# Kernel tuning notes

Measured on AMD Instinct MI355X. Metric: run time of the kernel, lower is better.

The kernel has to match this reference:

```python
import jax, jax.numpy as jnp
import numpy as np

BN_EPS = 1e-5

def _bn(h, gamma, beta):
    # training-mode BatchNorm1d over node dim, biased variance (as torch)
    m = jnp.mean(h, axis=0)
    v = jnp.var(h, axis=0)
    return (h - m) * jax.lax.rsqrt(v + BN_EPS) * gamma + beta

def _gin(x, edge_index, W, b, n_nodes):
    # PyG GINConv (eps=0): h = Linear(x + sum_{j in N(i)} x_j)
    src, dst = edge_index[0], edge_index[1]
    agg = jax.ops.segment_sum(x[src], dst, num_segments=n_nodes)
    return (x + agg) @ W + b

def setup_inputs() -> dict:
    key = jax.random.key(0)
    ks = jax.random.split(key, 16)
    N, E, D, H, G = 50000, 800000, 128, 256, 64
    x = jax.random.normal(ks[0], (N, D), dtype=jnp.float32)
    edge_index = jax.random.randint(ks[1], (2, E), 0, N, dtype=jnp.int64)
    batch = jnp.sort(jax.random.randint(ks[2], (N,), 0, G, dtype=jnp.int64))
    s = 0.05
    return {
        "x": x, "edge_index": edge_index, "batch": batch, "num_graphs": G,
        "W1": jax.random.normal(ks[3], (D, H), jnp.float32) * s,
        "b1": jnp.zeros((H,), jnp.float32),
        "W2": jax.random.normal(ks[4], (H, H), jnp.float32) * s,
        "b2": jnp.zeros((H,), jnp.float32),
        "W3": jax.random.normal(ks[5], (H, H), jnp.float32) * s,
        "b3": jnp.zeros((H,), jnp.float32),
        "g1": jnp.ones((H,), jnp.float32), "be1": jnp.zeros((H,), jnp.float32),
        "g2": jnp.ones((H,), jnp.float32), "be2": jnp.zeros((H,), jnp.float32),
        "g3": jnp.ones((H,), jnp.float32), "be3": jnp.zeros((H,), jnp.float32),
        "fcW1": jax.random.normal(ks[6], (H, H), jnp.float32) * s,
        "fcb1": jnp.zeros((H,), jnp.float32),
        "fcW2": jax.random.normal(ks[7], (H, 1), jnp.float32) * s,
        "fcb2": jnp.zeros((1,), jnp.float32),
    }

def reference(x, edge_index, batch, num_graphs, W1, b1, W2, b2, W3, b3,
              g1, be1, g2, be2, g3, be3, fcW1, fcb1, fcW2, fcb2):
    n_nodes = x.shape[0]
    # dropout treated as identity (eval / deterministic)
    x1 = jax.nn.relu(_bn(_gin(x, edge_index, W1, b1, n_nodes), g1, be1))
    x2 = jax.nn.relu(_bn(_gin(x1, edge_index, W2, b2, n_nodes), g2, be2)) + x1
    x3 = jax.nn.relu(_bn(_gin(x2, edge_index, W3, b3, n_nodes), g3, be3)) + x2
    # global mean pool over graphs
    sums = jax.ops.segment_sum(x3, batch, num_segments=num_graphs)
    cnt = jax.ops.segment_sum(jnp.ones((n_nodes,), x3.dtype), batch, num_segments=num_graphs)
    pooled = sums / jnp.maximum(cnt, 1.0)[:, None]
    h = jax.nn.relu(pooled @ fcW1 + fcb1)
    return h @ fcW2 + fcb2
```

## Files before the change

### kernel.cpp

```cpp
#include <hip/hip_runtime.h>
#include <hip/hip_bf16.h>
#include <stdint.h>

#define HDIM 256
#define NGRAPH 64

typedef short s16x8 __attribute__((ext_vector_type(8)));
typedef float f32x4 __attribute__((ext_vector_type(4)));

__device__ __forceinline__ float bf2f(unsigned short u){
    union { unsigned int i; float f; } x; x.i = ((unsigned int)u) << 16; return x.f;
}
__device__ __forceinline__ unsigned short f2bf(float f){
    union { float f; unsigned int i; } x; x.f = f;
    unsigned int r = x.i + 0x7fffu + ((x.i >> 16) & 1u);
    return (unsigned short)(r >> 16);
}
__device__ __forceinline__ float ldf(const void* p, int i, int f32){
    return f32 ? ((const float*)p)[i] : bf2f(((const unsigned short*)p)[i]);
}

__global__ void zero_detect_kernel(int* __restrict__ p, int n,
                                   const unsigned short* __restrict__ x,
                                   const int* __restrict__ ei, const int* __restrict__ batch,
                                   int E, int N, int* __restrict__ flags){
    int i = blockIdx.x * 256 + threadIdx.x;
    if (i < n) p[i] = 0;
    if (i == 0){
        int c = 0;
        for (int k = 0; k < 128; k++){
            unsigned e = (x[2 * k] >> 7) & 0xFFu;
            if (e >= 100u && e <= 140u) c++;
        }
        flags[0] = (c < 96) ? 1 : 0;
        int z = (ei[2*E - 1] == 0) && (ei[2*E - 3] == 0) && (ei[2*E - 5] == 0) && (ei[2*E - 7] == 0);
        flags[1] = z ? 1 : 0;
        flags[2] = (batch[N - 1] == 0) ? 1 : 0;
    }
}

__global__ void hist_kernel(const int* __restrict__ ei, int E, int N,
                            const int* __restrict__ flags, int* __restrict__ deg){
    int e = blockIdx.x * 256 + threadIdx.x;
    if (e < E){
        int is64 = flags[1];
        int d = is64 ? ei[2 * E + 2 * e] : ei[E + e];
        if ((unsigned)d < (unsigned)N) atomicAdd(&deg[d], 1);
    }
}

__global__ void scan1_kernel(const int* __restrict__ deg, int N,
                             int* __restrict__ incl, int* __restrict__ bsums){
    __shared__ int sm[256];
    int t = threadIdx.x;
    int i = blockIdx.x * 256 + t;
    int v = (i < N) ? deg[i] : 0;
    sm[t] = v; __syncthreads();
    for (int off = 1; off < 256; off <<= 1){
        int tv = (t >= off) ? sm[t - off] : 0;
        __syncthreads();
        sm[t] += tv;
        __syncthreads();
    }
    if (i < N) incl[i] = sm[t];
    if (t == 255) bsums[blockIdx.x] = sm[255];
}

__global__ void scan23_kernel(const int* __restrict__ deg, int N, int E, int nb,
                              const int* __restrict__ bsums, int* __restrict__ rowptr){
    __shared__ int sm[256];
    int t = threadIdx.x;
    int bid = blockIdx.x;
    sm[t] = (t < nb && t < bid) ? bsums[t] : 0;
    __syncthreads();
    for (int s = 128; s > 0; s >>= 1){
        if (t < s) sm[t] += sm[t + s];
        __syncthreads();
    }
    int prefix = sm[0];
    int i = bid * 256 + t;
    if (i < N) rowptr[i] = rowptr[i] - deg[i] + prefix;
    if (i == 0) rowptr[N] = E;
}

__global__ void fill_kernel(const int* __restrict__ ei, int E, int N,
                            const int* __restrict__ flags,
                            const int* __restrict__ rowptr, int* __restrict__ fillc,
                            int* __restrict__ csr){
    int e = blockIdx.x * 256 + threadIdx.x;
    if (e < E){
        int is64 = flags[1];
        int d = is64 ? ei[2 * E + 2 * e] : ei[E + e];
        int s = is64 ? ei[2 * e]         : ei[e];
        if ((unsigned)d < (unsigned)N){
            int p = atomicAdd(&fillc[d], 1);
            csr[rowptr[d] + p] = s;
        }
    }
}

__global__ void prep_kernel(const void* __restrict__ W1, unsigned short* __restrict__ Wt1,
                            const void* __restrict__ W2, unsigned short* __restrict__ Wt2,
                            const void* __restrict__ W3, unsigned short* __restrict__ Wt3,
                            const void* __restrict__ x, unsigned short* __restrict__ Xc,
                            int nx8, const int* __restrict__ flags){
    int bid = blockIdx.x;
    int f32 = flags[0];
    if (bid < 640){
        const void* W; unsigned short* Wt; int K, base;
        if (bid < 128)      { W = W1; Wt = Wt1; K = 128; base = bid; }
        else if (bid < 384) { W = W2; Wt = Wt2; K = 256; base = bid - 128; }
        else                { W = W3; Wt = Wt3; K = 256; base = bid - 384; }
        int idx = base * 256 + threadIdx.x;
        int n = idx / K, k = idx - n * K;
        Wt[idx] = f2bf(ldf(W, k * 256 + n, f32));
    } else {
        int i = (bid - 640) * 256 + threadIdx.x;
        if (i >= nx8) return;
        int base = i * 8;
        unsigned short o[8];
        if (f32){
            const float* s = (const float*)x + base;
            float4 a = *(const float4*)s;
            float4 b = *(const float4*)(s + 4);
            o[0]=f2bf(a.x); o[1]=f2bf(a.y); o[2]=f2bf(a.z); o[3]=f2bf(a.w);
            o[4]=f2bf(b.x); o[5]=f2bf(b.y); o[6]=f2bf(b.z); o[7]=f2bf(b.w);
        } else {
            *(uint4*)o = *(const uint4*)((const unsigned short*)x + base);
        }
        *(uint4*)&Xc[base] = *(uint4*)o;
    }
}

template<int C>
__global__ __launch_bounds__(256) void agg_vec(const unsigned short* __restrict__ feat, int ldi,
                                               const int* __restrict__ rowptr, const int* __restrict__ csr,
                                               unsigned short* __restrict__ Y, int ldo, int N){
    constexpr int L   = C / 8;
    constexpr int NPB = 256 / L;
    int node = blockIdx.x * NPB + threadIdx.x / L;
    int lane = threadIdx.x & (L - 1);
    if (node >= N) return;
    int c0 = lane * 8;
    const unsigned short* base = feat + c0;

    unsigned short t0[8];
    *(uint4*)t0 = *(const uint4*)&feat[(size_t)node * ldi + c0];
    float acc[8];
    #pragma unroll
    for (int j = 0; j < 8; j++) acc[j] = bf2f(t0[j]);

    int lo = rowptr[node], hi = rowptr[node + 1];
    int e = lo;
    for (; e + 3 < hi; e += 4){
        int s0 = csr[e], s1 = csr[e + 1], s2 = csr[e + 2], s3 = csr[e + 3];
        unsigned short ta[8], tb[8], tc[8], td[8];
        *(uint4*)ta = *(const uint4*)&base[(size_t)s0 * ldi];
        *(uint4*)tb = *(const uint4*)&base[(size_t)s1 * ldi];
        *(uint4*)tc = *(const uint4*)&base[(size_t)s2 * ldi];
        *(uint4*)td = *(const uint4*)&base[(size_t)s3 * ldi];
        #pragma unroll
        for (int j = 0; j < 8; j++)
            acc[j] += (bf2f(ta[j]) + bf2f(tb[j])) + (bf2f(tc[j]) + bf2f(td[j]));
    }
    for (; e < hi; e++){
        int s0 = csr[e];
        unsigned short ta[8];
        *(uint4*)ta = *(const uint4*)&base[(size_t)s0 * ldi];
        #pragma unroll
        for (int j = 0; j < 8; j++) acc[j] += bf2f(ta[j]);
    }
    unsigned short o[8];
    #pragma unroll
    for (int j = 0; j < 8; j++) o[j] = f2bf(acc[j]);
    *(uint4*)&Y[(size_t)node * ldo + c0] = *(uint4*)o;
}

__global__ __launch_bounds__(256) void gemm_tile(
    unsigned short* __restrict__ AC, int K,
    const unsigned short* __restrict__ Bt, const void* __restrict__ bias,
    int M, const int* __restrict__ flags,
    float* __restrict__ S, float* __restrict__ Q)
{
    __shared__ __align__(16) unsigned short As[64 * 72];
    __shared__ __align__(16) unsigned short Bs[256 * 72];
    __shared__ float sS[256], sQ[256];
    const int tid  = threadIdx.x;
    const int wave = tid >> 6, lane = tid & 63;
    const int quad = lane >> 4, l16 = lane & 15;
    const int m0   = blockIdx.x * 64;
    const int wn   = wave * 64;
    const bool full = (m0 + 64 <= M);
    const int f32  = flags[0];

    sS[tid] = 0.f; sQ[tid] = 0.f;

    const f32x4 zero4 = {0.f, 0.f, 0.f, 0.f};
    f32x4 acc[4][4];
    #pragma unroll
    for (int i = 0; i < 4; i++)
        #pragma unroll
        for (int j = 0; j < 4; j++) acc[i][j] = zero4;

    for (int kc = 0; kc < K; kc += 64){
        #pragma unroll
        for (int j = 0; j < 2; j++){
            int c = tid + j * 256;
            int r = c >> 3, cc = (c & 7) * 8;
            int gr = m0 + r;
            uint4 va; va.x = va.y = va.z = va.w = 0u;
            if (full || gr < M) va = *(const uint4*)&AC[(size_t)gr * HDIM + kc + cc];
            *(uint4*)&As[r * 72 + cc] = va;
        }
        #pragma unroll
        for (int j = 0; j < 8; j++){
            int c = tid + j * 256;
            int n = c >> 3, cc = (c & 7) * 8;
            *(uint4*)&Bs[n * 72 + cc] = *(const uint4*)&Bt[(size_t)n * K + kc + cc];
        }
        __syncthreads();
        #pragma unroll
        for (int kp = 0; kp < 64; kp += 32){
            s16x8 af[4], bfr[4];
            #pragma unroll
            for (int mt = 0; mt < 4; mt++)
                af[mt] = *(const s16x8*)&As[(mt * 16 + l16) * 72 + kp + quad * 8];
            #pragma unroll
            for (int nt = 0; nt < 4; nt++)
                bfr[nt] = *(const s16x8*)&Bs[(wn + nt * 16 + l16) * 72 + kp + quad * 8];
            #pragma unroll
            for (int mt = 0; mt < 4; mt++)
                #pragma unroll
                for (int nt = 0; nt < 4; nt++)
                    acc[mt][nt] = __builtin_amdgcn_mfma_f32_16x16x32_bf16(af[mt], bfr[nt], acc[mt][nt], 0, 0, 0);
        }
        __syncthreads();
    }
    #pragma unroll
    for (int nt = 0; nt < 4; nt++){
        int gc = wn + nt * 16 + l16;
        float bv = ldf(bias, gc, f32);
        float ps = 0.f, pq = 0.f;
        #pragma unroll
        for (int mt = 0; mt < 4; mt++){
            #pragma unroll
            for (int r = 0; r < 4; r++){
                int gr = m0 + mt * 16 + quad * 4 + r;
                if (full || gr < M){
                    float val = acc[mt][nt][r] + bv;
                    AC[(size_t)gr * HDIM + gc] = f2bf(val);
                    ps += val; pq += val * val;
                }
            }
        }
        atomicAdd(&sS[gc], ps);
        atomicAdd(&sQ[gc], pq);
    }
    __syncthreads();
    atomicAdd(&S[tid], sS[tid]);
    atomicAdd(&Q[tid], sQ[tid]);
}

__global__ void bnrelu_kernel(const unsigned short* __restrict__ Hin,
                              const float* __restrict__ S, const float* __restrict__ Q,
                              const void* __restrict__ g, const void* __restrict__ be,
                              float invM, const int* __restrict__ flags,
                              const unsigned short* __restrict__ res,
                              unsigned short* __restrict__ Out, int total16){
    __shared__ float sscale[256], sshift[256];
    int tid = threadIdx.x;
    {
        int f32 = flags[0];
        float m  = S[tid] * invM;
        float v  = Q[tid] * invM - m * m;
        float sc = ldf(g, tid, f32) * rsqrtf(v + 1e-5f);
        sscale[tid] = sc;
        sshift[tid] = ldf(be, tid, f32) - m * sc;
    }
    __syncthreads();
    int idx = blockIdx.x * 256 + tid;
    if (idx >= total16) return;
    #pragma unroll
    for (int h = 0; h < 2; h++){
        int base = idx * 16 + h * 8;
        int c = base & (HDIM - 1);
        unsigned short hv[8], rv[8], ov[8];
        *(uint4*)hv = *(const uint4*)&Hin[base];
        if (res) *(uint4*)rv = *(const uint4*)&res[base];
        #pragma unroll
        for (int j = 0; j < 8; j++){
            float v = bf2f(hv[j]) * sscale[c + j] + sshift[c + j];
            v = (v < 0.f) ? 0.f : v;
            if (res) v += bf2f(rv[j]);
            ov[j] = f2bf(v);
        }
        *(uint4*)&Out[base] = *(uint4*)ov;
    }
}

__global__ __launch_bounds__(256) void bnrelu_pool_kernel(
    const unsigned short* __restrict__ H, const unsigned short* __restrict__ res,
    const float* __restrict__ S, const float* __restrict__ Q,
    const void* __restrict__ g, const void* __restrict__ be,
    float invM, const int* __restrict__ flags,
    const int* __restrict__ batch, int N, float* __restrict__ sums)
{
    int r0 = blockIdx.x * 128;
    if (r0 >= N) return;
    int r1 = min(r0 + 128, N);
    int t = threadIdx.x;
    int f32 = flags[0];
    float m  = S[t] * invM;
    float v  = Q[t] * invM - m * m;
    float sc = ldf(g, t, f32) * rsqrtf(v + 1e-5f);
    float sh = ldf(be, t, f32) - m * sc;
    int stride = flags[2] ? 2 : 1;
    float acc = 0.f;
    int curg = batch[r0 * stride];
    for (int r = r0; r < r1; r++){
        int gg = batch[r * stride];
        if (gg != curg){
            atomicAdd(&sums[curg * HDIM + t], acc);
            acc = 0.f; curg = gg;
        }
        float hv = bf2f(H[(size_t)r * HDIM + t]) * sc + sh;
        hv = (hv < 0.f) ? 0.f : hv;
        hv += bf2f(res[(size_t)r * HDIM + t]);
        acc += hv;
    }
    atomicAdd(&sums[curg * HDIM + t], acc);
}

__global__ __launch_bounds__(256) void head_kernel(const float* __restrict__ sums,
                                                   const int* __restrict__ batch, int N,
                                                   const void* __restrict__ fcW1,
                                                   const void* __restrict__ fcb1,
                                                   const void* __restrict__ fcW2,
                                                   const void* __restrict__ fcb2,
                                                   void* __restrict__ out,
                                                   const int* __restrict__ flags){
    __shared__ float sp[256];
    __shared__ float red[256];
    __shared__ int scnt;
    int g = blockIdx.x, j = threadIdx.x;
    int f32 = flags[0];
    int stride = flags[2] ? 2 : 1;
    if (j == 0){
        int lo = 0, hi = N;
        while (lo < hi){ int mid = (lo + hi) >> 1; if (batch[mid * stride] < g) lo = mid + 1; else hi = mid; }
        int a = lo;
        lo = 0; hi = N;
        while (lo < hi){ int mid = (lo + hi) >> 1; if (batch[mid * stride] < g + 1) lo = mid + 1; else hi = mid; }
        scnt = lo - a;
    }
    __syncthreads();
    sp[j] = sums[g * HDIM + j] / (float)max(scnt, 1);
    __syncthreads();
    float acc = ldf(fcb1, j, f32);
    for (int k = 0; k < HDIM; k++) acc += sp[k] * ldf(fcW1, k * HDIM + j, f32);
    acc = (acc < 0.f) ? 0.f : acc;
    red[j] = acc * ldf(fcW2, j, f32);
    __syncthreads();
    for (int s = 128; s > 0; s >>= 1){
        if (j < s) red[j] += red[j + s];
        __syncthreads();
    }
    if (j == 0){
        float r = red[0] + ldf(fcb2, 0, f32);
        if (f32) ((float*)out)[g] = r;
        else     ((unsigned short*)out)[g] = f2bf(r);
    }
}

extern "C" void kernel_launch(void* const* d_in, const int* in_sizes, int n_in,
                              void* d_out, int out_size, void* d_ws, size_t ws_size,
                              hipStream_t stream)
{
    const unsigned short* x    = (const unsigned short*)d_in[0];
    const int*            ei   = (const int*)d_in[1];
    const int*            batch= (const int*)d_in[2];
    const void* W1   = d_in[4];
    const void* b1   = d_in[5];
    const void* W2   = d_in[6];
    const void* b2   = d_in[7];
    const void* W3   = d_in[8];
    const void* b3   = d_in[9];
    const void* g1   = d_in[10];
    const void* be1  = d_in[11];
    const void* g2   = d_in[12];
    const void* be2  = d_in[13];
    const void* g3   = d_in[14];
    const void* be3  = d_in[15];
    const void* fcW1 = d_in[16];
    const void* fcb1 = d_in[17];
    const void* fcW2 = d_in[18];
    const void* fcb2 = d_in[19];

    const int N = in_sizes[0] / 128;
    const int E = in_sizes[1] / 2;
    const int D = 128;

    char* p = (char*)d_ws;
    int*   deg     = (int*)p;   p += (size_t)N * 4;
    int*   fillc   = (int*)p;   p += (size_t)N * 4;
    float* stats   = (float*)p; p += 6 * 256 * 4;
    float* poolsum = (float*)p; p += NGRAPH * HDIM * 4;
    size_t zbytes  = (size_t)(p - (char*)d_ws);
    int*   flags   = (int*)p;   p += 16 * 4;
    int*   bsums   = (int*)p;   p += 256 * 4;
    int*   rowptr  = (int*)p;   p += ((size_t)N + 4) * 4;
    int*   csr     = (int*)p;   p += (size_t)E * 4;
    unsigned short* Wt1 = (unsigned short*)p; p += 256 * 128 * 2;
    unsigned short* Wt2 = (unsigned short*)p; p += 256 * 256 * 2;
    unsigned short* Wt3 = (unsigned short*)p; p += 256 * 256 * 2;
    unsigned short* B1  = (unsigned short*)p; p += (size_t)N * HDIM * 2;
    unsigned short* B2  = (unsigned short*)p; p += (size_t)N * HDIM * 2;
    unsigned short* Xc  = B1;

    float* S0 = stats + 0 * 256; float* Q0 = stats + 1 * 256;
    float* S1 = stats + 2 * 256; float* Q1 = stats + 3 * 256;
    float* S2 = stats + 4 * 256; float* Q2 = stats + 5 * 256;

    const int nbN = (N + 255) / 256;
    const int nbE = (E + 255) / 256;
    const int gM64  = (N + 63) / 64;
    const int gM128 = (N + 127) / 128;
    const float invM = 1.0f / (float)N;
    const int total16 = N * HDIM / 16;
    const int zn = (int)(zbytes / 4);
    const int nx8 = N * D / 8;

    zero_detect_kernel<<<(zn + 255) / 256, 256, 0, stream>>>((int*)d_ws, zn, x, ei, batch, E, N, flags);

    hist_kernel<<<nbE, 256, 0, stream>>>(ei, E, N, flags, deg);
    scan1_kernel<<<nbN, 256, 0, stream>>>(deg, N, rowptr, bsums);
    scan23_kernel<<<nbN, 256, 0, stream>>>(deg, N, E, nbN, bsums, rowptr);
    fill_kernel<<<nbE, 256, 0, stream>>>(ei, E, N, flags, rowptr, fillc, csr);

    prep_kernel<<<640 + (nx8 + 255) / 256, 256, 0, stream>>>(W1, Wt1, W2, Wt2, W3, Wt3, x, Xc, nx8, flags);

    agg_vec<128><<<(N + 15) / 16, 256, 0, stream>>>(Xc, D, rowptr, csr, B2, HDIM, N);
    gemm_tile<<<gM64, 256, 0, stream>>>(B2, 128, Wt1, b1, N, flags, S0, Q0);
    bnrelu_kernel<<<(total16 + 255) / 256, 256, 0, stream>>>(
        B2, S0, Q0, g1, be1, invM, flags, (const unsigned short*)nullptr, B1, total16);

    agg_vec<256><<<(N + 7) / 8, 256, 0, stream>>>(B1, HDIM, rowptr, csr, B2, HDIM, N);
    gemm_tile<<<gM64, 256, 0, stream>>>(B2, 256, Wt2, b2, N, flags, S1, Q1);
    bnrelu_kernel<<<(total16 + 255) / 256, 256, 0, stream>>>(
        B2, S1, Q1, g2, be2, invM, flags, B1, B1, total16);

    agg_vec<256><<<(N + 7) / 8, 256, 0, stream>>>(B1, HDIM, rowptr, csr, B2, HDIM, N);
    gemm_tile<<<gM64, 256, 0, stream>>>(B2, 256, Wt3, b3, N, flags, S2, Q2);
    bnrelu_pool_kernel<<<gM128, 256, 0, stream>>>(
        B2, B1, S2, Q2, g3, be3, invM, flags, batch, N, poolsum);

    head_kernel<<<NGRAPH, 256, 0, stream>>>(poolsum, batch, N, fcW1, fcb1, fcW2, fcb2, d_out, flags);

    (void)n_in; (void)out_size; (void)ws_size;
}
```

Measured before the change: 639.2 us.

## Prepack weights per K-chunk, shrink GEMM tiles, add nontemporal accesses, split aggregation

Weights are now prepacked into contiguous 32-wide K chunks so each GEMM block copies B with unit-stride loads, and the K step drops from 64 to 32 with unpadded shared memory. Aggregation and GEMM outputs use nontemporal stores, and the GEMM A loads are nontemporal, to reduce cache pollution. Each aggregation launch is split into two half-range launches. Removing the LDS padding may cause bank conflicts, and halving the K chunk doubles the number of barriers per tile.

```diff
diff --git a/kernel.cpp b/kernel.cpp
--- a/kernel.cpp
+++ b/kernel.cpp
@@ -7,6 +7,9 @@
 
 typedef short s16x8 __attribute__((ext_vector_type(8)));
 typedef float f32x4 __attribute__((ext_vector_type(4)));
+typedef unsigned int u32x4 __attribute__((ext_vector_type(4)));
+
+union U8 { u32x4 v; unsigned short s[8]; };
 
 __device__ __forceinline__ float bf2f(unsigned short u){
     union { unsigned int i; float f; } x; x.i = ((unsigned int)u) << 16; return x.f;
@@ -99,21 +102,23 @@
     }
 }
 
-__global__ void prep_kernel(const void* __restrict__ W1, unsigned short* __restrict__ Wt1,
-                            const void* __restrict__ W2, unsigned short* __restrict__ Wt2,
-                            const void* __restrict__ W3, unsigned short* __restrict__ Wt3,
+__global__ void prep_kernel(const void* __restrict__ W1, unsigned short* __restrict__ Wp1,
+                            const void* __restrict__ W2, unsigned short* __restrict__ Wp2,
+                            const void* __restrict__ W3, unsigned short* __restrict__ Wp3,
                             const void* __restrict__ x, unsigned short* __restrict__ Xc,
                             int nx8, const int* __restrict__ flags){
     int bid = blockIdx.x;
     int f32 = flags[0];
     if (bid < 640){
-        const void* W; unsigned short* Wt; int K, base;
-        if (bid < 128)      { W = W1; Wt = Wt1; K = 128; base = bid; }
-        else if (bid < 384) { W = W2; Wt = Wt2; K = 256; base = bid - 128; }
-        else                { W = W3; Wt = Wt3; K = 256; base = bid - 384; }
+        const void* W; unsigned short* Wp; int base;
+        if (bid < 128)      { W = W1; Wp = Wp1; base = bid; }
+        else if (bid < 384) { W = W2; Wp = Wp2; base = bid - 128; }
+        else                { W = W3; Wp = Wp3; base = bid - 384; }
         int idx = base * 256 + threadIdx.x;
-        int n = idx / K, k = idx - n * K;
-        Wt[idx] = f2bf(ldf(W, k * 256 + n, f32));
+        int k2 = idx & 31;
+        int nn = (idx >> 5) & 255;
+        int kc = idx >> 13;
+        Wp[idx] = f2bf(ldf(W, (kc * 32 + k2) * 256 + nn, f32));
     } else {
         int i = (bid - 640) * 256 + threadIdx.x;
         if (i >= nx8) return;
@@ -135,55 +140,54 @@
 template<int C>
 __global__ __launch_bounds__(256) void agg_vec(const unsigned short* __restrict__ feat, int ldi,
                                                const int* __restrict__ rowptr, const int* __restrict__ csr,
-                                               unsigned short* __restrict__ Y, int ldo, int N){
+                                               unsigned short* __restrict__ Y, int ldo,
+                                               int n0, int n1){
     constexpr int L   = C / 8;
     constexpr int NPB = 256 / L;
-    int node = blockIdx.x * NPB + threadIdx.x / L;
+    int node = n0 + blockIdx.x * NPB + threadIdx.x / L;
     int lane = threadIdx.x & (L - 1);
-    if (node >= N) return;
+    if (node >= n1) return;
     int c0 = lane * 8;
     const unsigned short* base = feat + c0;
 
-    unsigned short t0[8];
-    *(uint4*)t0 = *(const uint4*)&feat[(size_t)node * ldi + c0];
+    U8 t0; t0.v = *(const u32x4*)&feat[(size_t)node * ldi + c0];
     float acc[8];
     #pragma unroll
-    for (int j = 0; j < 8; j++) acc[j] = bf2f(t0[j]);
+    for (int j = 0; j < 8; j++) acc[j] = bf2f(t0.s[j]);
 
     int lo = rowptr[node], hi = rowptr[node + 1];
     int e = lo;
     for (; e + 3 < hi; e += 4){
         int s0 = csr[e], s1 = csr[e + 1], s2 = csr[e + 2], s3 = csr[e + 3];
-        unsigned short ta[8], tb[8], tc[8], td[8];
-        *(uint4*)ta = *(const uint4*)&base[(size_t)s0 * ldi];
-        *(uint4*)tb = *(const uint4*)&base[(size_t)s1 * ldi];
-        *(uint4*)tc = *(const uint4*)&base[(size_t)s2 * ldi];
-        *(uint4*)td = *(const uint4*)&base[(size_t)s3 * ldi];
+        U8 ta, tb, tc, td;
+        ta.v = *(const u32x4*)&base[(size_t)s0 * ldi];
+        tb.v = *(const u32x4*)&base[(size_t)s1 * ldi];
+        tc.v = *(const u32x4*)&base[(size_t)s2 * ldi];
+        td.v = *(const u32x4*)&base[(size_t)s3 * ldi];
         #pragma unroll
         for (int j = 0; j < 8; j++)
-            acc[j] += (bf2f(ta[j]) + bf2f(tb[j])) + (bf2f(tc[j]) + bf2f(td[j]));
+            acc[j] += (bf2f(ta.s[j]) + bf2f(tb.s[j])) + (bf2f(tc.s[j]) + bf2f(td.s[j]));
     }
     for (; e < hi; e++){
         int s0 = csr[e];
-        unsigned short ta[8];
-        *(uint4*)ta = *(const uint4*)&base[(size_t)s0 * ldi];
-        #pragma unroll
-        for (int j = 0; j < 8; j++) acc[j] += bf2f(ta[j]);
-    }
-    unsigned short o[8];
+        U8 ta; ta.v = *(const u32x4*)&base[(size_t)s0 * ldi];
+        #pragma unroll
+        for (int j = 0; j < 8; j++) acc[j] += bf2f(ta.s[j]);
+    }
+    U8 o;
     #pragma unroll
-    for (int j = 0; j < 8; j++) o[j] = f2bf(acc[j]);
-    *(uint4*)&Y[(size_t)node * ldo + c0] = *(uint4*)o;
+    for (int j = 0; j < 8; j++) o.s[j] = f2bf(acc[j]);
+    __builtin_nontemporal_store(o.v, (u32x4*)&Y[(size_t)node * ldo + c0]);
 }
 
 __global__ __launch_bounds__(256) void gemm_tile(
     unsigned short* __restrict__ AC, int K,
-    const unsigned short* __restrict__ Bt, const void* __restrict__ bias,
+    const unsigned short* __restrict__ Bp, const void* __restrict__ bias,
     int M, const int* __restrict__ flags,
     float* __restrict__ S, float* __restrict__ Q)
 {
-    __shared__ __align__(16) unsigned short As[64 * 72];
-    __shared__ __align__(16) unsigned short Bs[256 * 72];
+    __shared__ __align__(16) unsigned short As[64 * 32];
+    __shared__ __align__(16) unsigned short Bs[256 * 32];
     __shared__ float sS[256], sQ[256];
     const int tid  = threadIdx.x;
     const int wave = tid >> 6, lane = tid & 63;
@@ -202,38 +206,38 @@
         #pragma unroll
         for (int j = 0; j < 4; j++) acc[i][j] = zero4;
 
-    for (int kc = 0; kc < K; kc += 64){
-        #pragma unroll
-        for (int j = 0; j < 2; j++){
-            int c = tid + j * 256;
-            int r = c >> 3, cc = (c & 7) * 8;
+    const int nchunk = K >> 5;
+    for (int kc8 = 0; kc8 < nchunk; kc8++){
+        int kc = kc8 * 32;
+        {
+            int r = tid >> 2, cc = (tid & 3) * 8;
             int gr = m0 + r;
-            uint4 va; va.x = va.y = va.z = va.w = 0u;
-            if (full || gr < M) va = *(const uint4*)&AC[(size_t)gr * HDIM + kc + cc];
-            *(uint4*)&As[r * 72 + cc] = va;
-        }
-        #pragma unroll
-        for (int j = 0; j < 8; j++){
-            int c = tid + j * 256;
-            int n = c >> 3, cc = (c & 7) * 8;
-            *(uint4*)&Bs[n * 72 + cc] = *(const uint4*)&Bt[(size_t)n * K + kc + cc];
-        }
-        __syncthreads();
-        #pragma unroll
-        for (int kp = 0; kp < 64; kp += 32){
-            s16x8 af[4], bfr[4];
+            u32x4 va = {0u, 0u, 0u, 0u};
+            if (full || gr < M)
+                va = __builtin_nontemporal_load((const u32x4*)&AC[(size_t)gr * HDIM + kc + cc]);
+            *(u32x4*)&As[r * 32 + cc] = va;
+        }
+        {
+            const unsigned short* bc = Bp + (size_t)kc8 * 8192;
             #pragma unroll
-            for (int mt = 0; mt < 4; mt++)
-                af[mt] = *(const s16x8*)&As[(mt * 16 + l16) * 72 + kp + quad * 8];
+            for (int j = 0; j < 4; j++){
+                int c = tid + j * 256;
+                *(u32x4*)&Bs[c * 8] = *(const u32x4*)&bc[c * 8];
+            }
+        }
+        __syncthreads();
+        s16x8 af[4], bfr[4];
+        #pragma unroll
+        for (int mt = 0; mt < 4; mt++)
+            af[mt] = *(const s16x8*)&As[(mt * 16 + l16) * 32 + quad * 8];
+        #pragma unroll
+        for (int nt = 0; nt < 4; nt++)
+            bfr[nt] = *(const s16x8*)&Bs[(wn + nt * 16 + l16) * 32 + quad * 8];
+        #pragma unroll
+        for (int mt = 0; mt < 4; mt++)
             #pragma unroll
             for (int nt = 0; nt < 4; nt++)
-                bfr[nt] = *(const s16x8*)&Bs[(wn + nt * 16 + l16) * 72 + kp + quad * 8];
-            #pragma unroll
-            for (int mt = 0; mt < 4; mt++)
-                #pragma unroll
-                for (int nt = 0; nt < 4; nt++)
-                    acc[mt][nt] = __builtin_amdgcn_mfma_f32_16x16x32_bf16(af[mt], bfr[nt], acc[mt][nt], 0, 0, 0);
-        }
+                acc[mt][nt] = __builtin_amdgcn_mfma_f32_16x16x32_bf16(af[mt], bfr[nt], acc[mt][nt], 0, 0, 0);
         __syncthreads();
     }
     #pragma unroll
@@ -248,7 +252,7 @@
                 int gr = m0 + mt * 16 + quad * 4 + r;
                 if (full || gr < M){
                     float val = acc[mt][nt][r] + bv;
-                    AC[(size_t)gr * HDIM + gc] = f2bf(val);
+                    __builtin_nontemporal_store(f2bf(val), &AC[(size_t)gr * HDIM + gc]);
                     ps += val; pq += val * val;
                 }
             }
@@ -410,9 +414,9 @@
     int*   bsums   = (int*)p;   p += 256 * 4;
     int*   rowptr  = (int*)p;   p += ((size_t)N + 4) * 4;
     int*   csr     = (int*)p;   p += (size_t)E * 4;
-    unsigned short* Wt1 = (unsigned short*)p; p += 256 * 128 * 2;
-    unsigned short* Wt2 = (unsigned short*)p; p += 256 * 256 * 2;
-    unsigned short* Wt3 = (unsigned short*)p; p += 256 * 256 * 2;
+    unsigned short* Wp1 = (unsigned short*)p; p += 256 * 128 * 2;
+    unsigned short* Wp2 = (unsigned short*)p; p += 256 * 256 * 2;
+    unsigned short* Wp3 = (unsigned short*)p; p += 256 * 256 * 2;
     unsigned short* B1  = (unsigned short*)p; p += (size_t)N * HDIM * 2;
     unsigned short* B2  = (unsigned short*)p; p += (size_t)N * HDIM * 2;
     unsigned short* Xc  = B1;
@@ -429,6 +433,7 @@
     const int total16 = N * HDIM / 16;
     const int zn = (int)(zbytes / 4);
     const int nx8 = N * D / 8;
+    const int half = N / 2;
 
     zero_detect_kernel<<<(zn + 255) / 256, 256, 0, stream>>>((int*)d_ws, zn, x, ei, batch, E, N, flags);
 
@@ -437,20 +442,23 @@
     scan23_kernel<<<nbN, 256, 0, stream>>>(deg, N, E, nbN, bsums, rowptr);
     fill_kernel<<<nbE, 256, 0, stream>>>(ei, E, N, flags, rowptr, fillc, csr);
 
-    prep_kernel<<<640 + (nx8 + 255) / 256, 256, 0, stream>>>(W1, Wt1, W2, Wt2, W3, Wt3, x, Xc, nx8, flags);
-
-    agg_vec<128><<<(N + 15) / 16, 256, 0, stream>>>(Xc, D, rowptr, csr, B2, HDIM, N);
-    gemm_tile<<<gM64, 256, 0, stream>>>(B2, 128, Wt1, b1, N, flags, S0, Q0);
+    prep_kernel<<<640 + (nx8 + 255) / 256, 256, 0, stream>>>(W1, Wp1, W2, Wp2, W3, Wp3, x, Xc, nx8, flags);
+
+    agg_vec<128><<<(half + 15) / 16, 256, 0, stream>>>(Xc, D, rowptr, csr, B2, HDIM, 0, half);
+    agg_vec<128><<<(N - half + 15) / 16, 256, 0, stream>>>(Xc, D, rowptr, csr, B2, HDIM, half, N);
+    gemm_tile<<<gM64, 256, 0, stream>>>(B2, 128, Wp1, b1, N, flags, S0, Q0);
     bnrelu_kernel<<<(total16 + 255) / 256, 256, 0, stream>>>(
         B2, S0, Q0, g1, be1, invM, flags, (const unsigned short*)nullptr, B1, total16);
 
-    agg_vec<256><<<(N + 7) / 8, 256, 0, stream>>>(B1, HDIM, rowptr, csr, B2, HDIM, N);
-    gemm_tile<<<gM64, 256, 0, stream>>>(B2, 256, Wt2, b2, N, flags, S1, Q1);
+    agg_vec<256><<<(half + 7) / 8, 256, 0, stream>>>(B1, HDIM, rowptr, csr, B2, HDIM, 0, half);
+    agg_vec<256><<<(N - half + 7) / 8, 256, 0, stream>>>(B1, HDIM, rowptr, csr, B2, HDIM, half, N);
+    gemm_tile<<<gM64, 256, 0, stream>>>(B2, 256, Wp2, b2, N, flags, S1, Q1);
     bnrelu_kernel<<<(total16 + 255) / 256, 256, 0, stream>>>(
         B2, S1, Q1, g2, be2, invM, flags, B1, B1, total16);
 
-    agg_vec<256><<<(N + 7) / 8, 256, 0, stream>>>(B1, HDIM, rowptr, csr, B2, HDIM, N);
-    gemm_tile<<<gM64, 256, 0, stream>>>(B2, 256, Wt3, b3, N, flags, S2, Q2);
+    agg_vec<256><<<(half + 7) / 8, 256, 0, stream>>>(B1, HDIM, rowptr, csr, B2, HDIM, 0, half);
+    agg_vec<256><<<(N - half + 7) / 8, 256, 0, stream>>>(B1, HDIM, rowptr, csr, B2, HDIM, half, N);
+    gemm_tile<<<gM64, 256, 0, stream>>>(B2, 256, Wp3, b3, N, flags, S2, Q2);
     bnrelu_pool_kernel<<<gM128, 256, 0, stream>>>(
         B2, B1, S2, Q2, g3, be3, invM, flags, batch, N, poolsum);
 
```

Measured after the change: 704.3 us. 1.1x slower.
